# Kernel tuning notes

Measured on AMD Instinct MI355X. Metric: run time of the kernel, lower is better.

Reference implementation:

```python
import jax, jax.numpy as jnp
import numpy as np

SOS = 1

def setup_inputs() -> dict:
    key = jax.random.key(0)
    ks = jax.random.split(key, 12)
    B, S, T, H, V = 64, 128, 32, 1024, 32000
    sc = 0.02
    return {
        'encoder_outputs': jax.random.normal(ks[0], (B, S, H), jnp.float32),
        'encoder_hidden': jax.random.normal(ks[1], (1, B, H), jnp.float32),
        'target_tensor': jax.random.randint(ks[2], (B, T), 0, V),
        'embedding': jax.random.normal(ks[3], (V, H), jnp.float32) * sc,
        'Wa': jax.random.normal(ks[4], (H, H), jnp.float32) * sc,
        'ba': jnp.zeros((H,), jnp.float32),
        'Ua': jax.random.normal(ks[5], (H, H), jnp.float32) * sc,
        'bu': jnp.zeros((H,), jnp.float32),
        'Va': jax.random.normal(ks[6], (1, H), jnp.float32) * sc,
        'bv': jnp.zeros((1,), jnp.float32),
        'W_ih': jax.random.normal(ks[7], (3 * H, 2 * H), jnp.float32) * sc,
        'b_ih': jnp.zeros((3 * H,), jnp.float32),
        'W_hh': jax.random.normal(ks[8], (3 * H, H), jnp.float32) * sc,
        'b_hh': jnp.zeros((3 * H,), jnp.float32),
        'W_out': jax.random.normal(ks[9], (V, H), jnp.float32) * sc,
        'b_out': jnp.zeros((V,), jnp.float32),
    }

def reference(encoder_outputs, encoder_hidden, target_tensor, embedding,
              Wa, ba, Ua, bu, Va, bv, W_ih, b_ih, W_hh, b_hh, W_out, b_out):
    B, S, H = encoder_outputs.shape
    T = target_tensor.shape[1]
    # teacher forcing: input at step i is SOS for i=0 else target[:, i-1]
    tokens = jnp.concatenate([jnp.full((B, 1), SOS, target_tensor.dtype),
                              target_tensor[:, :-1]], axis=1)  # (B,T)
    emb = embedding[tokens]  # (B,T,H); dropout is identity (eval)
    keys_proj = jnp.einsum('bsh,gh->bsg', encoder_outputs, Ua) + bu  # Ua(keys), (B,S,H)
    h0 = encoder_hidden[0]  # (B,H)

    def step(h, x_t):
        # Bahdanau attention: Va(tanh(Wa q + Ua k))
        q = h @ Wa.T + ba  # (B,H)
        scores = jnp.einsum('bsh,h->bs', jnp.tanh(q[:, None, :] + keys_proj), Va[0]) + bv[0]
        w = jax.nn.softmax(scores, axis=-1)  # (B,S)
        ctx = jnp.einsum('bs,bsh->bh', w, encoder_outputs)
        x = jnp.concatenate([x_t, ctx], axis=-1)  # (B,2H)
        # GRU cell (PyTorch convention)
        gi = x @ W_ih.T + b_ih
        gh = h @ W_hh.T + b_hh
        ir, iz, inn = jnp.split(gi, 3, axis=-1)
        hr, hz, hn = jnp.split(gh, 3, axis=-1)
        r = jax.nn.sigmoid(ir + hr)
        z = jax.nn.sigmoid(iz + hz)
        n = jnp.tanh(inn + r * hn)
        h_new = (1.0 - z) * n + z * h
        logits = h_new @ W_out.T + b_out  # (B,V)
        return h_new, (logits, w)

    h_final, (logits, weights) = jax.lax.scan(step, h0, jnp.swapaxes(emb, 0, 1))
    log_probs = jax.nn.log_softmax(jnp.swapaxes(logits, 0, 1), axis=-1)  # (B,T,V)
    attentions = jnp.swapaxes(weights, 0, 1)  # (B,T,S)
    return log_probs, h_final[None], attentions
```

## Files before the change

### kernel.cpp

```cpp
#include <hip/hip_runtime.h>


typedef unsigned short u16;
typedef __bf16 bf16x8 __attribute__((ext_vector_type(8)));
typedef float f32x4 __attribute__((ext_vector_type(4)));
typedef u16 u16x8 __attribute__((ext_vector_type(8)));

#define DEV __device__ __forceinline__

DEV u16 f2b(float f) {
  union { float f; unsigned u; } v; v.f = f;
  unsigned r = v.u + 0x7fffu + ((v.u >> 16) & 1u);
  return (u16)(r >> 16);
}
DEV float b2f(u16 b) {
  union { unsigned u; float f; } v; v.u = ((unsigned)b) << 16;
  return v.f;
}
DEV float sigm(float x) { return 1.f / (1.f + __expf(-x)); }
DEV float ftanh(float x) {
  x = fminf(fmaxf(x, -20.f), 20.f);
  float e = __expf(2.f * x);
  return (e - 1.f) / (e + 1.f);
}
DEV void gl16(const void* g, void* l) {
  __builtin_amdgcn_global_load_lds((const __attribute__((address_space(1))) void*)g,
                                   (__attribute__((address_space(3))) void*)l, 16, 0, 0);
}

__global__ __launch_bounds__(256) void cvtall(const float* __restrict__ enc, const float* __restrict__ Ua,
                                              const float* __restrict__ Wa, const float* __restrict__ Whh,
                                              const float* __restrict__ Wout, u16* __restrict__ enc_b,
                                              u16* __restrict__ Ua_b, u16* __restrict__ Wa_b,
                                              u16* __restrict__ Whh_b, u16* __restrict__ Wout_b) {
  const long q_enc = 2097152;
  const long q_ua = q_enc + 262144;
  const long q_wa = q_ua + 262144;
  const long q_whh = q_wa + 786432;
  const long total = q_whh + 8192000;
  long stride = (long)gridDim.x * 256;
  for (long i = (long)blockIdx.x * 256 + threadIdx.x; i < total; i += stride) {
    const float* src; u16* dst; long off;
    if (i < q_enc) { src = enc; dst = enc_b; off = i; }
    else if (i < q_ua) { src = Ua; dst = Ua_b; off = i - q_enc; }
    else if (i < q_wa) { src = Wa; dst = Wa_b; off = i - q_ua; }
    else if (i < q_whh) { src = Whh; dst = Whh_b; off = i - q_wa; }
    else { src = Wout; dst = Wout_b; off = i - q_whh; }
    float4 v = ((const float4*)src)[off];
    ushort4 o; o.x = f2b(v.x); o.y = f2b(v.y); o.z = f2b(v.z); o.w = f2b(v.w);
    ((ushort4*)dst)[off] = o;
  }
}

__global__ __launch_bounds__(256) void cvtsplitk(const float* __restrict__ in, u16* __restrict__ o1,
                                                 u16* __restrict__ o2) {
  const long n4 = (long)3072 * 2048 / 4;
  long stride = (long)gridDim.x * 256;
  for (long i = (long)blockIdx.x * 256 + threadIdx.x; i < n4; i += stride) {
    long e = i * 4;
    int row = (int)(e >> 11), col = (int)(e & 2047);
    float4 v = ((const float4*)in)[i];
    ushort4 o; o.x = f2b(v.x); o.y = f2b(v.y); o.z = f2b(v.z); o.w = f2b(v.w);
    u16* dst = (col < 1024) ? (o1 + (size_t)row * 1024 + col) : (o2 + (size_t)row * 1024 + col - 1024);
    *(ushort4*)dst = o;
  }
}

__global__ __launch_bounds__(256) void embk(const float* __restrict__ embd, const int* __restrict__ tgt,
                                            u16* __restrict__ out) {
  int i = blockIdx.x * 256 + threadIdx.x;
  size_t e = (size_t)i * 4;
  int h = (int)(e & 1023);
  int bt = (int)(e >> 10);
  int b = bt >> 5, t = bt & 31;
  int tok = (t == 0) ? 1 : tgt[b * 32 + t - 1];
  const float* src = embd + (size_t)tok * 1024 + h;
  ushort4 o; o.x = f2b(src[0]); o.y = f2b(src[1]); o.z = f2b(src[2]); o.w = f2b(src[3]);
  *(ushort4*)(out + e) = o;
}

__global__ __launch_bounds__(256) void hinitk(const float* __restrict__ eh, float* __restrict__ hf,
                                              u16* __restrict__ hb) {
  int i = blockIdx.x * 256 + threadIdx.x;
  float v = eh[i];
  hf[i] = v; hb[i] = f2b(v);
}

template <int MODE>
__global__ __launch_bounds__(256) void gemm_tile(const u16* __restrict__ A, const u16* __restrict__ Bm,
                                                 const float* __restrict__ bias, float* __restrict__ Cf,
                                                 u16* __restrict__ Cb, int K, int ldc, int nTM) {
  __shared__ __attribute__((aligned(16))) u16 As[128 * 32];
  __shared__ __attribute__((aligned(16))) u16 Bs[128 * 32];
  const int tid = threadIdx.x, lane = tid & 63, w = tid >> 6;
  const int chunk = gridDim.x >> 3, wg = blockIdx.x;
  const int id = (wg & 7) * chunk + (wg >> 3);
  const int m = id % nTM, n = id / nTM;
  const int m0 = m * 128, n0 = n * 128;
  const int wm = w >> 1, wn = w & 1;
  const int l16 = lane & 15, kg = lane >> 4;
  const int srow = lane >> 2;
  const int skk = (((lane & 3) ^ ((srow >> 1) & 3)) * 8);
  const int slot = (kg ^ ((l16 >> 1) & 3)) * 8;

  f32x4 acc[4][4];
#pragma unroll
  for (int i = 0; i < 4; ++i)
#pragma unroll
    for (int j = 0; j < 4; ++j) acc[i][j] = f32x4{0.f, 0.f, 0.f, 0.f};

  for (int k0 = 0; k0 < K; k0 += 32) {
#pragma unroll
    for (int ch = 0; ch < 2; ++ch) {
      int c = w + ch * 4;
      gl16(A + (size_t)(m0 + c * 16 + srow) * K + k0 + skk, &As[c * 512]);
      gl16(Bm + (size_t)(n0 + c * 16 + srow) * K + k0 + skk, &Bs[c * 512]);
    }
    __syncthreads();
    bf16x8 av[4], bv[4];
#pragma unroll
    for (int i = 0; i < 4; ++i) av[i] = *(const bf16x8*)&As[(wm * 4 + i) * 512 + l16 * 32 + slot];
#pragma unroll
    for (int j = 0; j < 4; ++j) bv[j] = *(const bf16x8*)&Bs[(wn * 4 + j) * 512 + l16 * 32 + slot];
#pragma unroll
    for (int i = 0; i < 4; ++i)
#pragma unroll
      for (int j = 0; j < 4; ++j)
        acc[i][j] = __builtin_amdgcn_mfma_f32_16x16x32_bf16(av[i], bv[j], acc[i][j], 0, 0, 0);
    __syncthreads();
  }
#pragma unroll
  for (int i = 0; i < 4; ++i) {
    int rowb = m0 + (wm * 4 + i) * 16 + kg * 4;
#pragma unroll
    for (int j = 0; j < 4; ++j) {
      int col = n0 + (wn * 4 + j) * 16 + l16;
      float bb = bias[col];
#pragma unroll
      for (int r = 0; r < 4; ++r) {
        int row = rowb + r;
        float v = acc[i][j][r] + bb;
        if (MODE == 0) Cf[(size_t)row * ldc + col] = v;
        else Cb[(size_t)row * ldc + col] = f2b(v);
      }
    }
  }
}

template <int MODE>
__global__ __launch_bounds__(256, 2) void gemm_wide(const u16* __restrict__ A, const u16* __restrict__ Bm,
                                                    const float* __restrict__ bias, float* __restrict__ Cf,
                                                    u16* __restrict__ Cb, int K, int ldc) {
  __shared__ __attribute__((aligned(16))) u16 As[128 * 32];
  __shared__ __attribute__((aligned(16))) u16 Bs[256 * 32];
  const int tid = threadIdx.x, lane = tid & 63, w = tid >> 6;
  const int chunk = gridDim.x >> 3, wg = blockIdx.x;
  const int id = (wg & 7) * chunk + (wg >> 3);
  const int r_ = id % 80;
  const int m = r_ & 15, n = 5 * (id / 80) + (r_ >> 4);
  const int m0 = m * 128, n0 = n * 256;
  const int wm = w >> 1, wn = w & 1;
  const int l16 = lane & 15, kg = lane >> 4;
  const int srow = lane >> 2;
  const int skk = (((lane & 3) ^ ((srow >> 1) & 3)) * 8);
  const int slot = (kg ^ ((l16 >> 1) & 3)) * 8;

  f32x4 acc[4][8];
#pragma unroll
  for (int i = 0; i < 4; ++i)
#pragma unroll
    for (int j = 0; j < 8; ++j) acc[i][j] = f32x4{0.f, 0.f, 0.f, 0.f};

  for (int k0 = 0; k0 < K; k0 += 32) {
#pragma unroll
    for (int ch = 0; ch < 2; ++ch) {
      int c = w + ch * 4;
      gl16(A + (size_t)(m0 + c * 16 + srow) * K + k0 + skk, &As[c * 512]);
    }
#pragma unroll
    for (int ch = 0; ch < 4; ++ch) {
      int c = w + ch * 4;
      gl16(Bm + (size_t)(n0 + c * 16 + srow) * K + k0 + skk, &Bs[c * 512]);
    }
    __syncthreads();
    bf16x8 av[4], bv[8];
#pragma unroll
    for (int i = 0; i < 4; ++i) av[i] = *(const bf16x8*)&As[(wm * 4 + i) * 512 + l16 * 32 + slot];
#pragma unroll
    for (int j = 0; j < 8; ++j) bv[j] = *(const bf16x8*)&Bs[(wn * 8 + j) * 512 + l16 * 32 + slot];
#pragma unroll
    for (int i = 0; i < 4; ++i)
#pragma unroll
      for (int j = 0; j < 8; ++j)
        acc[i][j] = __builtin_amdgcn_mfma_f32_16x16x32_bf16(av[i], bv[j], acc[i][j], 0, 0, 0);
    __syncthreads();
  }
#pragma unroll
  for (int i = 0; i < 4; ++i) {
    int rowb = m0 + (wm * 4 + i) * 16 + kg * 4;
#pragma unroll
    for (int j = 0; j < 8; ++j) {
      int col = n0 + (wn * 8 + j) * 16 + l16;
      float bb = bias[col];
#pragma unroll
      for (int r = 0; r < 4; ++r) {
        int row = rowb + r;
        float v = acc[i][j][r] + bb;
        int b_ = row & 63, t_ = row >> 6;
        size_t ro = ((size_t)b_ * 32 + t_) * ldc + col;
        if (MODE == 0) Cf[ro] = v; else Cb[ro] = f2b(v);
      }
    }
  }
}

__global__ __launch_bounds__(256) void qkghk(const u16* __restrict__ hb, const u16* __restrict__ W1,
                                             float* __restrict__ qghp) {
  const int tid = threadIdx.x, lane = tid & 63, w = tid >> 6;
  const int l16 = lane & 15, kg = lane >> 4;
  const int pg = blockIdx.x >> 2, ks = blockIdx.x & 3;
  const u16* ap = hb + (size_t)(w * 16 + l16) * 1024 + ks * 256 + kg * 8;
  const u16* bp = W1 + (size_t)(pg * 16 + l16) * 1024 + ks * 256 + kg * 8;
  f32x4 a = {0.f, 0.f, 0.f, 0.f};
#pragma unroll
  for (int k0 = 0; k0 < 256; k0 += 32)
    a = __builtin_amdgcn_mfma_f32_16x16x32_bf16(*(const bf16x8*)(ap + k0), *(const bf16x8*)(bp + k0),
                                                a, 0, 0, 0);
  const int col = pg * 16 + l16;
#pragma unroll
  for (int r = 0; r < 4; ++r) {
    int b = w * 16 + kg * 4 + r;
    qghp[(size_t)ks * 262144 + b * 4096 + col] = a[r];
  }
}

__global__ __launch_bounds__(256) void scorekq(const float* __restrict__ qghp, const float* __restrict__ ba,
                                               const float* __restrict__ Va, const u16* __restrict__ kp,
                                               float* __restrict__ sc) {
  const int b = blockIdx.x >> 2, sq = blockIdx.x & 3;
  const int tid = threadIdx.x, lane = tid & 63, w = tid >> 6;
  __shared__ float qs[1024], vas[1024];
#pragma unroll
  for (int j = 0; j < 4; ++j) {
    int e = tid + j * 256;
    qs[e] = qghp[b * 4096 + e] + qghp[262144 + b * 4096 + e] + qghp[524288 + b * 4096 + e] +
            qghp[786432 + b * 4096 + e] + ba[e];
    vas[e] = Va[e];
  }
  __syncthreads();
#pragma unroll
  for (int si = 0; si < 8; ++si) {
    int s = sq * 32 + w * 8 + si;
    const bf16x8* kv = (const bf16x8*)(kp + ((size_t)b * 128 + s) * 1024);
    float a = 0.f;
#pragma unroll
    for (int i2 = 0; i2 < 2; ++i2) {
      int e = lane + 64 * i2;
      bf16x8 k8 = kv[e];
#pragma unroll
      for (int j = 0; j < 8; ++j) a += vas[e * 8 + j] * ftanh(qs[e * 8 + j] + (float)k8[j]);
    }
#pragma unroll
    for (int off = 32; off; off >>= 1) a += __shfl_xor(a, off);
    if (lane == 0) sc[b * 128 + s] = a;
  }
}

__global__ __launch_bounds__(256) void wsumgate(const float* __restrict__ scb, const u16* __restrict__ encW2,
                                                const float* __restrict__ gie, const float* __restrict__ qghp,
                                                const float* __restrict__ bhh, float* __restrict__ hf,
                                                u16* __restrict__ hbW, u16* __restrict__ hall,
                                                float* __restrict__ hfin, float* __restrict__ att_out, int t) {
  const int b = blockIdx.x >> 2, cg = blockIdx.x & 3;
  const int tid = threadIdx.x, lane = tid & 63, w = tid >> 6;
  __shared__ float wsm[128];
  if (w == 0) {
    float v0 = scb[b * 128 + lane], v1 = scb[b * 128 + 64 + lane];
    float mx = fmaxf(v0, v1);
#pragma unroll
    for (int off = 32; off; off >>= 1) mx = fmaxf(mx, __shfl_xor(mx, off));
    float e0 = __expf(v0 - mx), e1 = __expf(v1 - mx);
    float sm = e0 + e1;
#pragma unroll
    for (int off = 32; off; off >>= 1) sm += __shfl_xor(sm, off);
    float inv = 1.f / sm;
    e0 *= inv; e1 *= inv;
    wsm[lane] = e0; wsm[lane + 64] = e1;
    if (cg == 0) {
      size_t ao = ((size_t)b * 32 + t) * 128;
      att_out[ao + lane] = e0;
      att_out[ao + lane + 64] = e1;
    }
  }
  __syncthreads();
  const int col = cg * 256 + tid;
  float a0 = 0.f, a1 = 0.f, a2 = 0.f;
  const u16* ep = encW2 + (size_t)b * 128 * 3072 + col;
#pragma unroll 8
  for (int s = 0; s < 128; ++s) {
    float ws = wsm[s];
    a0 += ws * b2f(ep[0]);
    a1 += ws * b2f(ep[1024]);
    a2 += ws * b2f(ep[2048]);
    ep += 3072;
  }
  const float* ge = gie + ((size_t)b * 32 + t) * 3072 + col;
  const float* qg = qghp + (size_t)b * 4096 + 1024 + col;
  float hr = qg[0] + qg[262144] + qg[524288] + qg[786432] + bhh[col];
  float hz = qg[1024] + qg[1024 + 262144] + qg[1024 + 524288] + qg[1024 + 786432] + bhh[col + 1024];
  float hn = qg[2048] + qg[2048 + 262144] + qg[2048 + 524288] + qg[2048 + 786432] + bhh[col + 2048];
  float rr = sigm(a0 + ge[0] + hr);
  float zz = sigm(a1 + ge[1024] + hz);
  float nn = ftanh(a2 + ge[2048] + rr * hn);
  const int i = b * 1024 + col;
  float hp = hf[i];
  float hv = (1.f - zz) * nn + zz * hp;
  hf[i] = hv;
  u16 h16 = f2b(hv);
  hbW[i] = h16;
  hall[((size_t)t * 64 + b) * 1024 + col] = h16;
  if (t == 31) hfin[i] = hv;
}

__global__ __launch_bounds__(256) void smaxctxk(const float* __restrict__ sc, const u16* __restrict__ encb,
                                                u16* __restrict__ ctxb, float* __restrict__ att_out, int t) {
  const int b = blockIdx.x >> 2, hq = blockIdx.x & 3;
  const int tid = threadIdx.x, lane = tid & 63, w = tid >> 6;
  __shared__ float wsm[128];
  if (w == 0) {
    float v0 = sc[b * 128 + lane], v1 = sc[b * 128 + 64 + lane];
    float mx = fmaxf(v0, v1);
#pragma unroll
    for (int off = 32; off; off >>= 1) mx = fmaxf(mx, __shfl_xor(mx, off));
    float e0 = __expf(v0 - mx), e1 = __expf(v1 - mx);
    float sm = e0 + e1;
#pragma unroll
    for (int off = 32; off; off >>= 1) sm += __shfl_xor(sm, off);
    float inv = 1.f / sm;
    e0 *= inv; e1 *= inv;
    wsm[lane] = e0; wsm[lane + 64] = e1;
    if (hq == 0) {
      size_t ao = ((size_t)b * 32 + t) * 128;
      att_out[ao + lane] = e0;
      att_out[ao + lane + 64] = e1;
    }
  }
  __syncthreads();
  const int h = hq * 256 + tid;
  const u16* ep = encb + (size_t)b * 131072 + h;
  float c = 0.f;
#pragma unroll 8
  for (int s = 0; s < 128; ++s) c += wsm[s] * b2f(ep[(size_t)s * 1024]);
  ctxb[(size_t)b * 1024 + h] = f2b(c);
}

__global__ __launch_bounds__(256) void gi2w(const u16* __restrict__ ctxb, const u16* __restrict__ Wih2,
                                            float* __restrict__ gic) {
  const int tid = threadIdx.x, lane = tid & 63, w = tid >> 6;
  const int l16 = lane & 15, kg = lane >> 4;
  const int c0 = blockIdx.x * 16;
  const u16* ap = ctxb + (size_t)(w * 16 + l16) * 1024 + kg * 8;
  const u16* bp = Wih2 + (size_t)(c0 + l16) * 1024 + kg * 8;
  f32x4 a0 = {0.f, 0.f, 0.f, 0.f}, a1 = {0.f, 0.f, 0.f, 0.f};
#pragma unroll 4
  for (int k0 = 0; k0 < 1024; k0 += 64) {
    a0 = __builtin_amdgcn_mfma_f32_16x16x32_bf16(*(const bf16x8*)(ap + k0), *(const bf16x8*)(bp + k0),
                                                 a0, 0, 0, 0);
    a1 = __builtin_amdgcn_mfma_f32_16x16x32_bf16(*(const bf16x8*)(ap + k0 + 32),
                                                 *(const bf16x8*)(bp + k0 + 32), a1, 0, 0, 0);
  }
  const int col = c0 + l16;
#pragma unroll
  for (int r = 0; r < 4; ++r) {
    int b = w * 16 + kg * 4 + r;
    gic[(size_t)b * 3072 + col] = a0[r] + a1[r];
  }
}

__global__ __launch_bounds__(256) void gatesq(const float* __restrict__ gic, const float* __restrict__ gie,
                                              const float* __restrict__ qghp, const float* __restrict__ bhh,
                                              float* __restrict__ hf, u16* __restrict__ hbW,
                                              u16* __restrict__ hall, float* __restrict__ hfin, int t) {
  const int i = blockIdx.x * 256 + threadIdx.x;
  const int b = i >> 10, col = i & 1023;
  const float* gi = gic + (size_t)b * 3072 + col;
  const float* ge = gie + ((size_t)b * 32 + t) * 3072 + col;
  const float* qg = qghp + (size_t)b * 4096 + 1024 + col;
  float hr = qg[0] + qg[262144] + qg[524288] + qg[786432] + bhh[col];
  float hz = qg[1024] + qg[1024 + 262144] + qg[1024 + 524288] + qg[1024 + 786432] + bhh[col + 1024];
  float hn = qg[2048] + qg[2048 + 262144] + qg[2048 + 524288] + qg[2048 + 786432] + bhh[col + 2048];
  float rr = sigm(gi[0] + ge[0] + hr);
  float zz = sigm(gi[1024] + ge[1024] + hz);
  float nn = ftanh(gi[2048] + ge[2048] + rr * hn);
  float hp = hf[i];
  float hv = (1.f - zz) * nn + zz * hp;
  hf[i] = hv;
  u16 h16 = f2b(hv);
  hbW[i] = h16;
  hall[((size_t)t * 64 + b) * 1024 + col] = h16;
  if (t == 31) hfin[i] = hv;
}

__global__ __launch_bounds__(256) void logsoftk(const u16* __restrict__ lg, float* __restrict__ out) {
  const int row = blockIdx.x, tid = threadIdx.x, lane = tid & 63, w = tid >> 6;
  const u16x8* p = (const u16x8*)(lg + (size_t)row * 32000);
  __shared__ float red[4];
  u16x8 d[16];
#pragma unroll
  for (int j = 0; j < 16; ++j) {
    int i = tid + j * 256;
    if (i < 4000) d[j] = p[i];
  }
  float mx = -3.0e38f;
#pragma unroll
  for (int j = 0; j < 16; ++j) {
    int i = tid + j * 256;
    if (i < 4000)
#pragma unroll
      for (int k = 0; k < 8; ++k) mx = fmaxf(mx, b2f(d[j][k]));
  }
#pragma unroll
  for (int off = 32; off; off >>= 1) mx = fmaxf(mx, __shfl_xor(mx, off));
  if (lane == 0) red[w] = mx;
  __syncthreads();
  mx = fmaxf(fmaxf(red[0], red[1]), fmaxf(red[2], red[3]));
  __syncthreads();
  float s = 0.f;
#pragma unroll
  for (int j = 0; j < 16; ++j) {
    int i = tid + j * 256;
    if (i < 4000)
#pragma unroll
      for (int k = 0; k < 8; ++k) s += __expf(b2f(d[j][k]) - mx);
  }
#pragma unroll
  for (int off = 32; off; off >>= 1) s += __shfl_xor(s, off);
  if (lane == 0) red[w] = s;
  __syncthreads();
  float c = mx + __logf(red[0] + red[1] + red[2] + red[3]);
  float* op = out + (size_t)row * 32000;
#pragma unroll
  for (int j = 0; j < 16; ++j) {
    int i = tid + j * 256;
    if (i < 4000) {
      f32x4 o0, o1;
#pragma unroll
      for (int k = 0; k < 4; ++k) { o0[k] = b2f(d[j][k]) - c; o1[k] = b2f(d[j][k + 4]) - c; }
      *(f32x4*)(op + i * 8) = o0;
      *(f32x4*)(op + i * 8 + 4) = o1;
    }
  }
}

__global__ __launch_bounds__(256) void rowstatk(const float* __restrict__ lp, float* __restrict__ c) {
  int row = blockIdx.x;
  const float4* p = (const float4*)(lp + (size_t)row * 32000);
  int tid = threadIdx.x, lane = tid & 63, w = tid >> 6;
  __shared__ float redm[4], reds[4];
  float mx = -3.0e38f;
  for (int i = tid; i < 8000; i += 256) {
    float4 v = p[i];
    mx = fmaxf(mx, fmaxf(fmaxf(v.x, v.y), fmaxf(v.z, v.w)));
  }
#pragma unroll
  for (int off = 32; off; off >>= 1) mx = fmaxf(mx, __shfl_xor(mx, off));
  if (lane == 0) redm[w] = mx;
  __syncthreads();
  mx = fmaxf(fmaxf(redm[0], redm[1]), fmaxf(redm[2], redm[3]));
  float s = 0.f;
  for (int i = tid; i < 8000; i += 256) {
    float4 v = p[i];
    s += __expf(v.x - mx) + __expf(v.y - mx) + __expf(v.z - mx) + __expf(v.w - mx);
  }
#pragma unroll
  for (int off = 32; off; off >>= 1) s += __shfl_xor(s, off);
  if (lane == 0) reds[w] = s;
  __syncthreads();
  if (tid == 0) c[row] = mx + __logf(reds[0] + reds[1] + reds[2] + reds[3]);
}

__global__ __launch_bounds__(256) void subk(float* __restrict__ lp, const float* __restrict__ c) {
  const long n4 = (long)64 * 32 * 32000 / 4;
  long stride = (long)gridDim.x * 256;
  for (long i = (long)blockIdx.x * 256 + threadIdx.x; i < n4; i += stride) {
    float4 v = ((float4*)lp)[i];
    float cc = c[i / 8000];
    v.x -= cc; v.y -= cc; v.z -= cc; v.w -= cc;
    ((float4*)lp)[i] = v;
  }
}

extern "C" void kernel_launch(void* const* d_in, const int* in_sizes, int n_in, void* d_out, int out_size,
                              void* d_ws, size_t ws_size, hipStream_t stream) {
  (void)in_sizes; (void)n_in; (void)out_size;
  constexpr int B = 64, S = 128, T = 32, H = 1024, V = 32000;

  const float* enc  = (const float*)d_in[0];
  const float* ehid = (const float*)d_in[1];
  const int*   tgt  = (const int*)d_in[2];
  const float* embd = (const float*)d_in[3];
  const float* Wa   = (const float*)d_in[4];
  const float* ba   = (const float*)d_in[5];
  const float* Ua   = (const float*)d_in[6];
  const float* bu   = (const float*)d_in[7];
  const float* Va   = (const float*)d_in[8];
  const float* Wih  = (const float*)d_in[10];
  const float* bih  = (const float*)d_in[11];
  const float* Whh  = (const float*)d_in[12];
  const float* bhh  = (const float*)d_in[13];
  const float* Wout = (const float*)d_in[14];
  const float* bout = (const float*)d_in[15];

  char* wp = (char*)d_ws;
  auto alloc = [&](size_t bytes) {
    char* p = wp;
    wp += (bytes + 255) & ~(size_t)255;
    return p;
  };
  u16* enc_b  = (u16*)alloc((size_t)B * S * H * 2);
  u16* kp_b   = (u16*)alloc((size_t)B * S * H * 2);
  u16* Ua_b   = (u16*)alloc((size_t)H * H * 2);
  u16* W1_b   = (u16*)alloc((size_t)4096 * 1024 * 2);
  u16* Wih1_b = (u16*)alloc((size_t)3072 * 1024 * 2);
  u16* Wih2_b = (u16*)alloc((size_t)3072 * 1024 * 2);
  u16* Wout_b = (u16*)alloc((size_t)V * H * 2);
  u16* emb_b  = (u16*)alloc((size_t)B * T * H * 2);
  u16* hall_b = (u16*)alloc((size_t)T * B * H * 2);
  float* gie  = (float*)alloc((size_t)B * T * 3072 * 4);
  float* qghp = (float*)alloc((size_t)4 * B * 4096 * 4);
  float* scb  = (float*)alloc((size_t)B * S * 4);
  float* gic  = (float*)alloc((size_t)B * 3072 * 4);
  u16* ctx_b  = (u16*)alloc((size_t)B * H * 2);
  u16* hb0    = (u16*)alloc((size_t)B * H * 2);
  u16* hb1    = (u16*)alloc((size_t)B * H * 2);
  float* h_f  = (float*)alloc((size_t)B * H * 4);
  float* rowc = (float*)alloc(2048 * 4);
  float* zbias = (float*)alloc(3072 * 4);
  size_t base_need = (size_t)(wp - (char*)d_ws);
  u16* encW2 = (u16*)alloc((size_t)B * S * 3072 * 2);
  bool have_w2 = ((size_t)(wp - (char*)d_ws) <= ws_size);
  u16* lg_b = (u16*)alloc((size_t)B * T * V * 2);
  bool bflog = ((size_t)(wp - (char*)d_ws) <= ws_size);
  if (base_need > ws_size) return;

  float* out_lp = (float*)d_out;
  float* out_hf = out_lp + (size_t)B * T * V;
  float* out_at = out_hf + (size_t)B * H;

  u16* Wa_slot = W1_b;
  u16* Whh_slot = W1_b + (size_t)1024 * 1024;
  cvtall<<<2048, 256, 0, stream>>>(enc, Ua, Wa, Whh, Wout, enc_b, Ua_b, Wa_slot, Whh_slot, Wout_b);
  cvtsplitk<<<2048, 256, 0, stream>>>(Wih, Wih1_b, Wih2_b);
  embk<<<2048, 256, 0, stream>>>(embd, tgt, emb_b);
  hinitk<<<256, 256, 0, stream>>>(ehid, h_f, hb0);

  gemm_tile<1><<<512, 256, 0, stream>>>(enc_b, Ua_b, bu, nullptr, kp_b, H, H, 64);
  gemm_tile<0><<<384, 256, 0, stream>>>(emb_b, Wih1_b, bih, gie, nullptr, H, 3072, 16);
  if (have_w2) {
    hipMemsetAsync(zbias, 0, 3072 * 4, stream);
    gemm_tile<1><<<1536, 256, 0, stream>>>(enc_b, Wih2_b, zbias, nullptr, encW2, H, 3072, 64);
  }

  for (int t = 0; t < T; ++t) {
    u16* hbR = (t & 1) ? hb1 : hb0;
    u16* hbW = (t & 1) ? hb0 : hb1;
    qkghk<<<1024, 256, 0, stream>>>(hbR, W1_b, qghp);
    scorekq<<<256, 256, 0, stream>>>(qghp, ba, Va, kp_b, scb);
    if (have_w2) {
      wsumgate<<<256, 256, 0, stream>>>(scb, encW2, gie, qghp, bhh, h_f, hbW, hall_b, out_hf, out_at, t);
    } else {
      smaxctxk<<<256, 256, 0, stream>>>(scb, enc_b, ctx_b, out_at, t);
      gi2w<<<192, 256, 0, stream>>>(ctx_b, Wih2_b, gic);
      gatesq<<<256, 256, 0, stream>>>(gic, gie, qghp, bhh, h_f, hbW, hall_b, out_hf, t);
    }
  }

  if (bflog) {
    gemm_wide<1><<<2000, 256, 0, stream>>>(hall_b, Wout_b, bout, nullptr, lg_b, H, V);
    logsoftk<<<2048, 256, 0, stream>>>(lg_b, out_lp);
  } else {
    gemm_wide<0><<<2000, 256, 0, stream>>>(hall_b, Wout_b, bout, out_lp, nullptr, H, V);
    rowstatk<<<2048, 256, 0, stream>>>(out_lp, rowc);
    subk<<<2048, 256, 0, stream>>>(out_lp, rowc);
  }
}
```

Baseline: 1.540 ms.

## Merge prep kernels, widen per-step score and gate kernels, drop zero-bias memset

The four preprocessing kernels (weight/encoder bf16 conversion, W_ih split, embedding gather, hidden init) become one grid-stride kernel, and the memset for the zero bias is removed through a new GEMM mode that skips the bias. In the per-timestep loop, the score kernel launches twice as many blocks with fewer sequence positions each. The weighted-sum/gate kernel uses 512 threads, splitting the sequence reduction into two halves that are combined through shared memory. Together these cut launch count and raise parallelism in the latency-bound recurrent steps, at the cost of an extra barrier and idle threads in the gate epilogue.

Result: faster. 1.425 ms (-7.5%).

```diff
diff --git a/kernel.cpp b/kernel.cpp
--- a/kernel.cpp
+++ b/kernel.cpp
@@ -28,62 +28,64 @@
                                    (__attribute__((address_space(3))) void*)l, 16, 0, 0);
 }
 
-__global__ __launch_bounds__(256) void cvtall(const float* __restrict__ enc, const float* __restrict__ Ua,
-                                              const float* __restrict__ Wa, const float* __restrict__ Whh,
-                                              const float* __restrict__ Wout, u16* __restrict__ enc_b,
-                                              u16* __restrict__ Ua_b, u16* __restrict__ Wa_b,
-                                              u16* __restrict__ Whh_b, u16* __restrict__ Wout_b) {
-  const long q_enc = 2097152;
-  const long q_ua = q_enc + 262144;
-  const long q_wa = q_ua + 262144;
-  const long q_whh = q_wa + 786432;
-  const long total = q_whh + 8192000;
+__global__ __launch_bounds__(256) void prepk(const float* __restrict__ enc, const float* __restrict__ Ua,
+                                             const float* __restrict__ Wa, const float* __restrict__ Whh,
+                                             const float* __restrict__ Wout, const float* __restrict__ Wih,
+                                             const float* __restrict__ embd, const int* __restrict__ tgt,
+                                             const float* __restrict__ eh, u16* __restrict__ enc_b,
+                                             u16* __restrict__ Ua_b, u16* __restrict__ Wa_b,
+                                             u16* __restrict__ Whh_b, u16* __restrict__ Wout_b,
+                                             u16* __restrict__ Wih1_b, u16* __restrict__ Wih2_b,
+                                             u16* __restrict__ emb_b, float* __restrict__ hf,
+                                             u16* __restrict__ hb0) {
+  const long q0 = 2097152;
+  const long q1 = q0 + 262144;
+  const long q2 = q1 + 262144;
+  const long q3 = q2 + 786432;
+  const long q4 = q3 + 8192000;
+  const long q5 = q4 + 1572864;
+  const long q6 = q5 + 524288;
+  const long q7 = q6 + 16384;
   long stride = (long)gridDim.x * 256;
-  for (long i = (long)blockIdx.x * 256 + threadIdx.x; i < total; i += stride) {
-    const float* src; u16* dst; long off;
-    if (i < q_enc) { src = enc; dst = enc_b; off = i; }
-    else if (i < q_ua) { src = Ua; dst = Ua_b; off = i - q_enc; }
-    else if (i < q_wa) { src = Wa; dst = Wa_b; off = i - q_ua; }
-    else if (i < q_whh) { src = Whh; dst = Whh_b; off = i - q_wa; }
-    else { src = Wout; dst = Wout_b; off = i - q_whh; }
-    float4 v = ((const float4*)src)[off];
-    ushort4 o; o.x = f2b(v.x); o.y = f2b(v.y); o.z = f2b(v.z); o.w = f2b(v.w);
-    ((ushort4*)dst)[off] = o;
-  }
-}
-
-__global__ __launch_bounds__(256) void cvtsplitk(const float* __restrict__ in, u16* __restrict__ o1,
-                                                 u16* __restrict__ o2) {
-  const long n4 = (long)3072 * 2048 / 4;
-  long stride = (long)gridDim.x * 256;
-  for (long i = (long)blockIdx.x * 256 + threadIdx.x; i < n4; i += stride) {
-    long e = i * 4;
-    int row = (int)(e >> 11), col = (int)(e & 2047);
-    float4 v = ((const float4*)in)[i];
-    ushort4 o; o.x = f2b(v.x); o.y = f2b(v.y); o.z = f2b(v.z); o.w = f2b(v.w);
-    u16* dst = (col < 1024) ? (o1 + (size_t)row * 1024 + col) : (o2 + (size_t)row * 1024 + col - 1024);
-    *(ushort4*)dst = o;
-  }
-}
-
-__global__ __launch_bounds__(256) void embk(const float* __restrict__ embd, const int* __restrict__ tgt,
-                                            u16* __restrict__ out) {
-  int i = blockIdx.x * 256 + threadIdx.x;
-  size_t e = (size_t)i * 4;
-  int h = (int)(e & 1023);
-  int bt = (int)(e >> 10);
-  int b = bt >> 5, t = bt & 31;
-  int tok = (t == 0) ? 1 : tgt[b * 32 + t - 1];
-  const float* src = embd + (size_t)tok * 1024 + h;
-  ushort4 o; o.x = f2b(src[0]); o.y = f2b(src[1]); o.z = f2b(src[2]); o.w = f2b(src[3]);
-  *(ushort4*)(out + e) = o;
-}
-
-__global__ __launch_bounds__(256) void hinitk(const float* __restrict__ eh, float* __restrict__ hf,
-                                              u16* __restrict__ hb) {
-  int i = blockIdx.x * 256 + threadIdx.x;
-  float v = eh[i];
-  hf[i] = v; hb[i] = f2b(v);
+  for (long i = (long)blockIdx.x * 256 + threadIdx.x; i < q7; i += stride) {
+    if (i < q4) {
+      const float* src; u16* dst; long off;
+      if (i < q0) { src = enc; dst = enc_b; off = i; }
+      else if (i < q1) { src = Ua; dst = Ua_b; off = i - q0; }
+      else if (i < q2) { src = Wa; dst = Wa_b; off = i - q1; }
+      else if (i < q3) { src = Whh; dst = Whh_b; off = i - q2; }
+      else { src = Wout; dst = Wout_b; off = i - q3; }
+      float4 v = ((const float4*)src)[off];
+      ushort4 o; o.x = f2b(v.x); o.y = f2b(v.y); o.z = f2b(v.z); o.w = f2b(v.w);
+      ((ushort4*)dst)[off] = o;
+    } else if (i < q5) {
+      long off = i - q4;
+      long e = off * 4;
+      int row = (int)(e >> 11), col = (int)(e & 2047);
+      float4 v = ((const float4*)Wih)[off];
+      ushort4 o; o.x = f2b(v.x); o.y = f2b(v.y); o.z = f2b(v.z); o.w = f2b(v.w);
+      u16* dst = (col < 1024) ? (Wih1_b + (size_t)row * 1024 + col)
+                              : (Wih2_b + (size_t)row * 1024 + col - 1024);
+      *(ushort4*)dst = o;
+    } else if (i < q6) {
+      long off = i - q5;
+      size_t e = (size_t)off * 4;
+      int h = (int)(e & 1023);
+      int bt = (int)(e >> 10);
+      int b = bt >> 5, t = bt & 31;
+      int tok = (t == 0) ? 1 : tgt[b * 32 + t - 1];
+      const float* src = embd + (size_t)tok * 1024 + h;
+      float4 v = *(const float4*)src;
+      ushort4 o; o.x = f2b(v.x); o.y = f2b(v.y); o.z = f2b(v.z); o.w = f2b(v.w);
+      *(ushort4*)(emb_b + e) = o;
+    } else {
+      long off = i - q6;
+      float4 v = ((const float4*)eh)[off];
+      ((float4*)hf)[off] = v;
+      ushort4 o; o.x = f2b(v.x); o.y = f2b(v.y); o.z = f2b(v.z); o.w = f2b(v.w);
+      ((ushort4*)hb0)[off] = o;
+    }
+  }
 }
 
 template <int MODE>
@@ -135,7 +137,7 @@
 #pragma unroll
     for (int j = 0; j < 4; ++j) {
       int col = n0 + (wn * 4 + j) * 16 + l16;
-      float bb = bias[col];
+      float bb = (MODE == 2) ? 0.f : bias[col];
 #pragma unroll
       for (int r = 0; r < 4; ++r) {
         int row = rowb + r;
@@ -237,7 +239,7 @@
 __global__ __launch_bounds__(256) void scorekq(const float* __restrict__ qghp, const float* __restrict__ ba,
                                                const float* __restrict__ Va, const u16* __restrict__ kp,
                                                float* __restrict__ sc) {
-  const int b = blockIdx.x >> 2, sq = blockIdx.x & 3;
+  const int b = blockIdx.x >> 3, s8 = blockIdx.x & 7;
   const int tid = threadIdx.x, lane = tid & 63, w = tid >> 6;
   __shared__ float qs[1024], vas[1024];
 #pragma unroll
@@ -249,8 +251,8 @@
   }
   __syncthreads();
 #pragma unroll
-  for (int si = 0; si < 8; ++si) {
-    int s = sq * 32 + w * 8 + si;
+  for (int si = 0; si < 4; ++si) {
+    int s = s8 * 16 + w * 4 + si;
     const bf16x8* kv = (const bf16x8*)(kp + ((size_t)b * 128 + s) * 1024);
     float a = 0.f;
 #pragma unroll
@@ -266,7 +268,7 @@
   }
 }
 
-__global__ __launch_bounds__(256) void wsumgate(const float* __restrict__ scb, const u16* __restrict__ encW2,
+__global__ __launch_bounds__(512) void wsumgate(const float* __restrict__ scb, const u16* __restrict__ encW2,
                                                 const float* __restrict__ gie, const float* __restrict__ qghp,
                                                 const float* __restrict__ bhh, float* __restrict__ hf,
                                                 u16* __restrict__ hbW, u16* __restrict__ hall,
@@ -274,6 +276,7 @@
   const int b = blockIdx.x >> 2, cg = blockIdx.x & 3;
   const int tid = threadIdx.x, lane = tid & 63, w = tid >> 6;
   __shared__ float wsm[128];
+  __shared__ float pa[3][2][256];
   if (w == 0) {
     float v0 = scb[b * 128 + lane], v1 = scb[b * 128 + 64 + lane];
     float mx = fmaxf(v0, v1);
@@ -293,33 +296,42 @@
     }
   }
   __syncthreads();
-  const int col = cg * 256 + tid;
+  const int ct = tid & 255, half = tid >> 8;
+  const int col = cg * 256 + ct;
   float a0 = 0.f, a1 = 0.f, a2 = 0.f;
-  const u16* ep = encW2 + (size_t)b * 128 * 3072 + col;
+  const u16* ep = encW2 + (size_t)b * 128 * 3072 + (size_t)half * 64 * 3072 + col;
 #pragma unroll 8
-  for (int s = 0; s < 128; ++s) {
-    float ws = wsm[s];
+  for (int s = 0; s < 64; ++s) {
+    float ws = wsm[half * 64 + s];
     a0 += ws * b2f(ep[0]);
     a1 += ws * b2f(ep[1024]);
     a2 += ws * b2f(ep[2048]);
     ep += 3072;
   }
-  const float* ge = gie + ((size_t)b * 32 + t) * 3072 + col;
-  const float* qg = qghp + (size_t)b * 4096 + 1024 + col;
-  float hr = qg[0] + qg[262144] + qg[524288] + qg[786432] + bhh[col];
-  float hz = qg[1024] + qg[1024 + 262144] + qg[1024 + 524288] + qg[1024 + 786432] + bhh[col + 1024];
-  float hn = qg[2048] + qg[2048 + 262144] + qg[2048 + 524288] + qg[2048 + 786432] + bhh[col + 2048];
-  float rr = sigm(a0 + ge[0] + hr);
-  float zz = sigm(a1 + ge[1024] + hz);
-  float nn = ftanh(a2 + ge[2048] + rr * hn);
-  const int i = b * 1024 + col;
-  float hp = hf[i];
-  float hv = (1.f - zz) * nn + zz * hp;
-  hf[i] = hv;
-  u16 h16 = f2b(hv);
-  hbW[i] = h16;
-  hall[((size_t)t * 64 + b) * 1024 + col] = h16;
-  if (t == 31) hfin[i] = hv;
+  pa[0][half][ct] = a0; pa[1][half][ct] = a1; pa[2][half][ct] = a2;
+  __syncthreads();
+  if (tid < 256) {
+    float g0 = pa[0][0][tid] + pa[0][1][tid];
+    float g1 = pa[1][0][tid] + pa[1][1][tid];
+    float g2 = pa[2][0][tid] + pa[2][1][tid];
+    const int c2 = cg * 256 + tid;
+    const float* ge = gie + ((size_t)b * 32 + t) * 3072 + c2;
+    const float* qg = qghp + (size_t)b * 4096 + 1024 + c2;
+    float hr = qg[0] + qg[262144] + qg[524288] + qg[786432] + bhh[c2];
+    float hz = qg[1024] + qg[1024 + 262144] + qg[1024 + 524288] + qg[1024 + 786432] + bhh[c2 + 1024];
+    float hn = qg[2048] + qg[2048 + 262144] + qg[2048 + 524288] + qg[2048 + 786432] + bhh[c2 + 2048];
+    float rr = sigm(g0 + ge[0] + hr);
+    float zz = sigm(g1 + ge[1024] + hz);
+    float nn = ftanh(g2 + ge[2048] + rr * hn);
+    const int i = b * 1024 + c2;
+    float hp = hf[i];
+    float hv = (1.f - zz) * nn + zz * hp;
+    hf[i] = hv;
+    u16 h16 = f2b(hv);
+    hbW[i] = h16;
+    hall[((size_t)t * 64 + b) * 1024 + c2] = h16;
+    if (t == 31) hfin[i] = hv;
+  }
 }
 
 __global__ __launch_bounds__(256) void smaxctxk(const float* __restrict__ sc, const u16* __restrict__ encb,
@@ -535,7 +547,6 @@
   u16* hb1    = (u16*)alloc((size_t)B * H * 2);
   float* h_f  = (float*)alloc((size_t)B * H * 4);
   float* rowc = (float*)alloc(2048 * 4);
-  float* zbias = (float*)alloc(3072 * 4);
   size_t base_need = (size_t)(wp - (char*)d_ws);
   u16* encW2 = (u16*)alloc((size_t)B * S * 3072 * 2);
   bool have_w2 = ((size_t)(wp - (char*)d_ws) <= ws_size);
@@ -549,25 +560,24 @@
 
   u16* Wa_slot = W1_b;
   u16* Whh_slot = W1_b + (size_t)1024 * 1024;
-  cvtall<<<2048, 256, 0, stream>>>(enc, Ua, Wa, Whh, Wout, enc_b, Ua_b, Wa_slot, Whh_slot, Wout_b);
-  cvtsplitk<<<2048, 256, 0, stream>>>(Wih, Wih1_b, Wih2_b);
-  embk<<<2048, 256, 0, stream>>>(embd, tgt, emb_b);
-  hinitk<<<256, 256, 0, stream>>>(ehid, h_f, hb0);
+  prepk<<<2048, 256, 0, stream>>>(enc, Ua, Wa, Whh, Wout, Wih, embd, tgt, ehid,
+                                  enc_b, Ua_b, Wa_slot, Whh_slot, Wout_b,
+                                  Wih1_b, Wih2_b, emb_b, h_f, hb0);
 
   gemm_tile<1><<<512, 256, 0, stream>>>(enc_b, Ua_b, bu, nullptr, kp_b, H, H, 64);
   gemm_tile<0><<<384, 256, 0, stream>>>(emb_b, Wih1_b, bih, gie, nullptr, H, 3072, 16);
   if (have_w2) {
-    hipMemsetAsync(zbias, 0, 3072 * 4, stream);
-    gemm_tile<1><<<1536, 256, 0, stream>>>(enc_b, Wih2_b, zbias, nullptr, encW2, H, 3072, 64);
+    gemm_tile<2><<<1536, 256, 0, stream>>>(enc_b, Wih2_b, nullptr, nullptr, encW2, H, 3072, 64);
   }
 
   for (int t = 0; t < T; ++t) {
     u16* hbR = (t & 1) ? hb1 : hb0;
     u16* hbW = (t & 1) ? hb0 : hb1;
     qkghk<<<1024, 256, 0, stream>>>(hbR, W1_b, qghp);
-    scorekq<<<256, 256, 0, stream>>>(qghp, ba, Va, kp_b, scb);
+    scorekq<<<512, 256, 0, stream>>>(qghp, ba, Va, kp_b, scb);
     if (have_w2) {
-      wsumgate<<<256, 256, 0, stream>>>(scb, encW2, gie, qghp, bhh, h_f, hbW, hall_b, out_hf, out_at, t);
+      wsumgate<<<256, 512, 0, stream>>>(scb, encW2, gie, qghp, bhh, h_f, hbW, hall_b,
+                                        out_hf, out_at, t);
     } else {
       smaxctxk<<<256, 256, 0, stream>>>(scb, enc_b, ctx_b, out_at, t);
       gi2w<<<192, 256, 0, stream>>>(ctx_b, Wih2_b, gic);
```
